# Kernel tuning notes

Measured on AMD Instinct MI355X. Metric: run time of the kernel, lower is better.

## Reference

```python
import jax, jax.numpy as jnp
import numpy as np

B, S, D, H = 1, 2048, 1024, 16
HD = D // H
S_SLOPE = 10.0      # soft_thres_layer s
C_MASK = -10000.0   # soft_thres_layer c == masked_bias
ALPHA = 0.0         # config.threshold
W_STD = 0.02        # GPT2 init std for weights


def setup_inputs() -> dict:
    key = jax.random.key(0)
    k1, k2, k3 = jax.random.split(key, 3)
    return {
        "hidden_states": jax.random.normal(k1, (B, S, D), dtype=jnp.float32),
        "c_attn_w": jax.random.normal(k2, (D, 3 * D), dtype=jnp.float32) * W_STD,
        "c_attn_b": jnp.zeros((3 * D,), dtype=jnp.float32),
        "c_proj_w": jax.random.normal(k3, (D, D), dtype=jnp.float32) * W_STD,
        "c_proj_b": jnp.zeros((D,), dtype=jnp.float32),
    }


def reference(hidden_states, c_attn_w, c_attn_b, c_proj_w, c_proj_b):
    # Conv1D: x @ w + b (GPT2 convention: weight is [in, out])
    qkv = hidden_states @ c_attn_w + c_attn_b            # [B,S,3D]
    q, k, v = jnp.split(qkv, 3, axis=-1)

    def split_heads(x):
        return x.reshape(B, S, H, HD).transpose(0, 2, 1, 3)  # [B,H,S,hd]

    q, k, v = split_heads(q), split_heads(k), split_heads(v)

    # prun path: NO 1/sqrt(d) scaling (skipped when self.prun is True)
    w = jnp.einsum("bhqd,bhkd->bhqk", q, k)              # [B,H,S,S]

    causal = jnp.tril(jnp.ones((S, S), dtype=bool))[None, None]
    w = jnp.where(causal, w, C_MASK)

    # soft-threshold pruning: smoothly pushes scores below alpha toward c=-10000
    w = C_MASK + (w - C_MASK) * jax.nn.sigmoid(S_SLOPE * (w - ALPHA))

    a = jax.nn.softmax(w, axis=-1)                        # attn_dropout = identity (eval)
    out = jnp.einsum("bhqk,bhkd->bhqd", a, v)             # [B,H,S,hd]
    out = out.transpose(0, 2, 1, 3).reshape(B, S, D)      # merge heads
    return out @ c_proj_w + c_proj_b                      # resid_dropout = identity
```

## Files before the change

### kernel.cpp

```cpp
#include <hip/hip_runtime.h>


#define S_LEN 2048
#define DM    1024
#define NH    16
#define HD    64
#define NQKV  3072
#define SLOPE 10.0f
#define CMASK -10000.0f

typedef short s16x4 __attribute__((ext_vector_type(4)));
typedef short s16x8 __attribute__((ext_vector_type(8)));
typedef float f32x4 __attribute__((ext_vector_type(4)));

#define MFMA16(a,b,c) __builtin_amdgcn_mfma_f32_16x16x32_bf16(a,b,c,0,0,0)
#define GLDS16(g,l) __builtin_amdgcn_global_load_lds( \
    (const __attribute__((address_space(1))) void*)(g), \
    (__attribute__((address_space(3))) void*)(l), 16, 0, 0)

__device__ __forceinline__ short f2bf(float f){
    unsigned u = __float_as_uint(f);
    u += 0x7fffu + ((u >> 16) & 1u);
    return (short)(u >> 16);
}
__device__ __forceinline__ float bf2f(short x){
    return __uint_as_float(((unsigned)(unsigned short)x) << 16);
}
struct bfpair { short hi, lo; };
__device__ __forceinline__ bfpair split_bf(float x){
    bfpair r; r.hi = f2bf(x);
    r.lo = f2bf(x - bf2f(r.hi));
    return r;
}

template<int ROWS, int THREADS>
__device__ __forceinline__ void stage_tile(const short* gbase, int rstride,
                                           short* lds, int tid){
#pragma unroll
    for (int it = 0; it < ROWS*8/THREADS; ++it){
        int s = it*THREADS + tid;
        int row = s >> 3, grp = s & 7;
        const short* src = gbase + (size_t)row*rstride + ((grp ^ (row & 7)) << 3);
        GLDS16(src, lds + (size_t)s*8);
    }
}
__device__ __forceinline__ s16x8 frag(const short* lds, int row, int kg){
    return *(const s16x8*)&lds[row*64 + ((kg ^ (row & 7)) << 3)];
}

template<bool WSPLIT, bool QKV>
__global__ __launch_bounds__(256)
void gemm_kern(const short* __restrict__ Ahg, const short* __restrict__ Alg,
               const short* __restrict__ Bhg, const short* __restrict__ Blg,
               const float* __restrict__ bias,
               short* __restrict__ o0h, short* __restrict__ o0l,
               short* __restrict__ o1h,
               short* __restrict__ o2,  float* __restrict__ oproj)
{
    __shared__ __align__(16) short Ah_s[128*64];
    __shared__ __align__(16) short Al_s[128*64];
    __shared__ __align__(16) short Bh_s[128*64];
    __shared__ __align__(16) short Bl_s[WSPLIT ? 128*64 : 8];

    const int tid = threadIdx.x, lane = tid & 63, wid = tid >> 6;
    const int lr = lane & 15, lg = lane >> 4;
    const int brow = blockIdx.y*128, bcol = blockIdx.x*128;
    const int wm = (wid >> 1)*64, wn = (wid & 1)*64;

    f32x4 acc[4][4];
#pragma unroll
    for (int m = 0; m < 4; ++m)
#pragma unroll
        for (int n = 0; n < 4; ++n) acc[m][n] = (f32x4){0.f,0.f,0.f,0.f};

    for (int k0 = 0; k0 < DM; k0 += 64){
        stage_tile<128,256>(Ahg + (size_t)brow*DM + k0, DM, Ah_s, tid);
        stage_tile<128,256>(Alg + (size_t)brow*DM + k0, DM, Al_s, tid);
        stage_tile<128,256>(Bhg + (size_t)bcol*DM + k0, DM, Bh_s, tid);
        if constexpr (WSPLIT)
            stage_tile<128,256>(Blg + (size_t)bcol*DM + k0, DM, Bl_s, tid);
        __syncthreads();
#pragma unroll
        for (int kc = 0; kc < 2; ++kc){
            s16x8 ah[4], al[4], bh[4], bl[4];
#pragma unroll
            for (int m = 0; m < 4; ++m){
                ah[m] = frag(Ah_s, wm + m*16 + lr, kc*4 + lg);
                al[m] = frag(Al_s, wm + m*16 + lr, kc*4 + lg);
            }
#pragma unroll
            for (int n = 0; n < 4; ++n){
                bh[n] = frag(Bh_s, wn + n*16 + lr, kc*4 + lg);
                if constexpr (WSPLIT)
                    bl[n] = frag(Bl_s, wn + n*16 + lr, kc*4 + lg);
            }
#pragma unroll
            for (int m = 0; m < 4; ++m)
#pragma unroll
                for (int n = 0; n < 4; ++n){
                    acc[m][n] = MFMA16(ah[m], bh[n], acc[m][n]);
                    if constexpr (WSPLIT)
                        acc[m][n] = MFMA16(ah[m], bl[n], acc[m][n]);
                    acc[m][n] = MFMA16(al[m], bh[n], acc[m][n]);
                }
        }
        __syncthreads();
    }

    const int sec = bcol >> 10;
#pragma unroll
    for (int m = 0; m < 4; ++m)
#pragma unroll
        for (int n = 0; n < 4; ++n){
            int row  = brow + wm + m*16 + lg*4;
            int gcol = bcol + wn + n*16 + lr;
            float bv = bias[gcol];
#pragma unroll
            for (int v = 0; v < 4; ++v){
                float val = acc[m][n][v] + bv;
                if constexpr (QKV){
                    int col1 = gcol & 1023;
                    size_t o = (size_t)(row + v)*DM + col1;
                    if (sec == 0){ bfpair p = split_bf(val); o0h[o] = p.hi; o0l[o] = p.lo; }
                    else if (sec == 1){ o1h[o] = f2bf(val); }
                    else { o2[o] = f2bf(val); }
                } else {
                    oproj[(size_t)(row + v)*DM + gcol] = val;
                }
            }
        }
}

__global__ __launch_bounds__(256)
void split_f32(const float* __restrict__ x, short* __restrict__ h,
               short* __restrict__ l, int n4)
{
    int i = blockIdx.x*256 + threadIdx.x;
    if (i >= n4) return;
    float4 v = *(const float4*)&x[(size_t)i*4];
    bfpair a = split_bf(v.x), b = split_bf(v.y), c = split_bf(v.z), d = split_bf(v.w);
    s16x4 hv, lv;
    hv.x = a.hi; hv.y = b.hi; hv.z = c.hi; hv.w = d.hi;
    lv.x = a.lo; lv.y = b.lo; lv.z = c.lo; lv.w = d.lo;
    *(s16x4*)&h[(size_t)i*4] = hv;
    *(s16x4*)&l[(size_t)i*4] = lv;
}

template<bool SPL>
__global__ __launch_bounds__(256)
void wtrans(const float* __restrict__ W, int N, short* __restrict__ Th,
            short* __restrict__ Tl)
{
    __shared__ float t[64][65];
    const int tid = threadIdx.x;
    const int tn = blockIdx.x*64, tk = blockIdx.y*64;
#pragma unroll
    for (int it = 0; it < 4; ++it){
        int idx = tid + it*256;
        int r = idx >> 4, c4 = (idx & 15)*4;
        float4 v = *(const float4*)&W[(size_t)(tk + r)*N + tn + c4];
        t[r][c4] = v.x; t[r][c4+1] = v.y; t[r][c4+2] = v.z; t[r][c4+3] = v.w;
    }
    __syncthreads();
#pragma unroll
    for (int it = 0; it < 4; ++it){
        int idx = tid + it*256;
        int n = idx >> 4, c4 = (idx & 15)*4;
        s16x4 hv, lv;
#pragma unroll
        for (int j = 0; j < 4; ++j){
            bfpair p = split_bf(t[c4+j][n]);
            hv[j] = p.hi; lv[j] = p.lo;
        }
        *(s16x4*)&Th[(size_t)(tn + n)*DM + tk + c4] = hv;
        if constexpr (SPL) *(s16x4*)&Tl[(size_t)(tn + n)*DM + tk + c4] = lv;
    }
}

__global__ __launch_bounds__(256)
void vtrans(const short* __restrict__ Vb, short* __restrict__ Vt)
{
    __shared__ short t[64][66];
    const int tid = threadIdx.x;
    const int td = blockIdx.x*64, ts = blockIdx.y*64;
#pragma unroll
    for (int it = 0; it < 4; ++it){
        int idx = tid + it*256;
        int r = idx >> 4, c4 = (idx & 15)*4;
        s16x4 v = *(const s16x4*)&Vb[(size_t)(ts + r)*DM + td + c4];
        t[r][c4] = v.x; t[r][c4+1] = v.y; t[r][c4+2] = v.z; t[r][c4+3] = v.w;
    }
    __syncthreads();
#pragma unroll
    for (int it = 0; it < 4; ++it){
        int idx = tid + it*256;
        int n = idx >> 4, c4 = (idx & 15)*4;
        s16x4 o;
#pragma unroll
        for (int j = 0; j < 4; ++j) o[j] = t[c4+j][n];
        *(s16x4*)&Vt[(size_t)(td + n)*S_LEN + ts + c4] = o;
    }
}

__global__ __launch_bounds__(64)
void sv_partial(const short* __restrict__ Vb, float* __restrict__ PB)
{
    int b = blockIdx.x, h = blockIdx.y, d = threadIdx.x;
    float s = 0.f;
#pragma unroll 8
    for (int k = 0; k < 64; ++k)
        s += bf2f(Vb[(size_t)(b*64 + k)*DM + h*HD + d]);
    PB[((size_t)h*32 + b)*64 + d] = s;
}
__global__ __launch_bounds__(64)
void sv_suffix(const float* __restrict__ PB, float* __restrict__ SSV)
{
    int h = blockIdx.x, d = threadIdx.x;
    float s = 0.f;
    SSV[((size_t)h*33 + 32)*64 + d] = 0.f;
    for (int b = 31; b >= 0; --b){
        s += PB[((size_t)h*32 + b)*64 + d];
        SSV[((size_t)h*33 + b)*64 + d] = s;
    }
}

__global__ __launch_bounds__(256)
void attn_fwd(const short* __restrict__ Qh, const short* __restrict__ Ql,
              const short* __restrict__ Kh, const short* __restrict__ Vt,
              const float* __restrict__ SSV,
              short* __restrict__ Oh, short* __restrict__ Ol)
{
    __shared__ __align__(16) short Ps[4][16*72];
    __shared__ float mrg[3][64][24];

    const int id = blockIdx.x;
    const int h  = (id & 7) + 8*((id >> 3) & 1);
    const int qt = 127 - (id >> 4);
    const int diag = qt >> 2;

    const int tid = threadIdx.x, lane = tid & 63, wid = tid >> 6;
    const int lr = lane & 15, lg = lane >> 4;
    const int qrow = qt*16 + lg*4;

    const short* qbh = Qh + (size_t)(qt*16)*DM + h*HD;
    const short* qbl = Ql + (size_t)(qt*16)*DM + h*HD;
    s16x8 aqh[2], aql[2];
#pragma unroll
    for (int kc = 0; kc < 2; ++kc){
        aqh[kc] = *(const s16x8*)&qbh[(size_t)lr*DM + kc*32 + lg*8];
        aql[kc] = *(const s16x8*)&qbl[(size_t)lr*DM + kc*32 + lg*8];
    }

    float m_run[4], l_run[4];
    f32x4 acc_o[4];
#pragma unroll
    for (int v = 0; v < 4; ++v){ m_run[v] = -1e30f; l_run[v] = 0.f; }
#pragma unroll
    for (int n = 0; n < 4; ++n) acc_o[n] = (f32x4){0.f,0.f,0.f,0.f};

    const short* kb0 = Kh + (size_t)h*HD;
    const short* vb0 = Vt + (size_t)(h*HD)*S_LEN;

    s16x8 bkc[2][4];
    if (wid <= diag){
        const short* kb = kb0 + (size_t)(wid*64)*DM;
#pragma unroll
        for (int kc = 0; kc < 2; ++kc)
#pragma unroll
            for (int n = 0; n < 4; ++n)
                bkc[kc][n] = *(const s16x8*)&kb[(size_t)(n*16 + lr)*DM + kc*32 + lg*8];
    }

    for (int kvb = wid; kvb <= diag; kvb += 4){
        s16x8 bkn[2][4];
        if (kvb + 4 <= diag){
            const short* kb = kb0 + (size_t)((kvb+4)*64)*DM;
#pragma unroll
            for (int kc = 0; kc < 2; ++kc)
#pragma unroll
                for (int n = 0; n < 4; ++n)
                    bkn[kc][n] = *(const s16x8*)&kb[(size_t)(n*16 + lr)*DM + kc*32 + lg*8];
        }

        f32x4 sc[4];
#pragma unroll
        for (int n = 0; n < 4; ++n) sc[n] = (f32x4){0.f,0.f,0.f,0.f};
#pragma unroll
        for (int kc = 0; kc < 2; ++kc)
#pragma unroll
            for (int n = 0; n < 4; ++n){
                sc[n] = MFMA16(aqh[kc], bkc[kc][n], sc[n]);
                sc[n] = MFMA16(aql[kc], bkc[kc][n], sc[n]);
            }

        const short* vb = vb0 + kvb*64;
        s16x8 bv0[4], bv1[4];
#pragma unroll
        for (int n = 0; n < 4; ++n){
            bv0[n] = *(const s16x8*)&vb[(size_t)(16*n + lr)*S_LEN + lg*8];
            bv1[n] = *(const s16x8*)&vb[(size_t)(16*n + lr)*S_LEN + 32 + lg*8];
        }

        float p[4][4], tmax[4];
#pragma unroll
        for (int v = 0; v < 4; ++v) tmax[v] = -1e30f;
        if (kvb == diag){
#pragma unroll
            for (int n = 0; n < 4; ++n){
                int key = kvb*64 + n*16 + lr;
#pragma unroll
                for (int v = 0; v < 4; ++v){
                    float w;
                    if (key > qrow + v) w = CMASK;
                    else {
                        float sv = sc[n][v];
                        float sig = 1.f / (1.f + __expf(-SLOPE*sv));
                        w = CMASK + (sv - CMASK)*sig;
                    }
                    p[n][v] = w;
                    tmax[v] = fmaxf(tmax[v], w);
                }
            }
        } else {
#pragma unroll
            for (int n = 0; n < 4; ++n)
#pragma unroll
                for (int v = 0; v < 4; ++v){
                    float sv = sc[n][v];
                    float sig = 1.f / (1.f + __expf(-SLOPE*sv));
                    float w = CMASK + (sv - CMASK)*sig;
                    p[n][v] = w;
                    tmax[v] = fmaxf(tmax[v], w);
                }
        }
#pragma unroll
        for (int v = 0; v < 4; ++v)
#pragma unroll
            for (int msk = 1; msk < 16; msk <<= 1)
                tmax[v] = fmaxf(tmax[v], __shfl_xor(tmax[v], msk, 64));

        float scale[4], rsum[4];
#pragma unroll
        for (int v = 0; v < 4; ++v){
            float mn = fmaxf(m_run[v], tmax[v]);
            scale[v] = __expf(m_run[v] - mn);
            m_run[v] = mn;
            rsum[v] = 0.f;
        }
#pragma unroll
        for (int n = 0; n < 4; ++n)
#pragma unroll
            for (int v = 0; v < 4; ++v){
                float e = __expf(p[n][v] - m_run[v]);
                p[n][v] = e;
                rsum[v] += e;
            }
#pragma unroll
        for (int v = 0; v < 4; ++v){
#pragma unroll
            for (int msk = 1; msk < 16; msk <<= 1)
                rsum[v] += __shfl_xor(rsum[v], msk, 64);
            l_run[v] = l_run[v]*scale[v] + rsum[v];
        }
#pragma unroll
        for (int n = 0; n < 4; ++n)
#pragma unroll
            for (int v = 0; v < 4; ++v) acc_o[n][v] *= scale[v];

#pragma unroll
        for (int n = 0; n < 4; ++n)
#pragma unroll
            for (int v = 0; v < 4; ++v)
                Ps[wid][(lg*4 + v)*72 + 16*n + lr] = f2bf(p[n][v]);
        asm volatile("s_waitcnt lgkmcnt(0)" ::: "memory");

        s16x8 pa0 = *(const s16x8*)&Ps[wid][lr*72 + lg*8];
        s16x8 pa1 = *(const s16x8*)&Ps[wid][lr*72 + 32 + lg*8];
#pragma unroll
        for (int n = 0; n < 4; ++n){
            acc_o[n] = MFMA16(pa0, bv0[n], acc_o[n]);
            acc_o[n] = MFMA16(pa1, bv1[n], acc_o[n]);
        }

#pragma unroll
        for (int kc = 0; kc < 2; ++kc)
#pragma unroll
            for (int n = 0; n < 4; ++n) bkc[kc][n] = bkn[kc][n];
    }

    if (wid != 0){
#pragma unroll
        for (int v = 0; v < 4; ++v){
            mrg[wid-1][lane][v] = m_run[v];
            mrg[wid-1][lane][4 + v] = l_run[v];
        }
#pragma unroll
        for (int n = 0; n < 4; ++n)
#pragma unroll
            for (int v = 0; v < 4; ++v) mrg[wid-1][lane][8 + n*4 + v] = acc_o[n][v];
    }
    __syncthreads();
    if (wid != 0) return;

#pragma unroll
    for (int w = 0; w < 3; ++w){
        float e0[4], e1[4];
#pragma unroll
        for (int v = 0; v < 4; ++v){
            float m1 = mrg[w][lane][v], l1 = mrg[w][lane][4 + v];
            float mn = fmaxf(m_run[v], m1);
            e0[v] = __expf(m_run[v] - mn);
            e1[v] = __expf(m1 - mn);
            l_run[v] = l_run[v]*e0[v] + l1*e1[v];
            m_run[v] = mn;
        }
#pragma unroll
        for (int n = 0; n < 4; ++n)
#pragma unroll
            for (int v = 0; v < 4; ++v)
                acc_o[n][v] = acc_o[n][v]*e0[v] + mrg[w][lane][8 + n*4 + v]*e1[v];
    }

    {
        const float* sv = SSV + ((size_t)h*33 + (diag + 1))*64;
        float F = (float)(S_LEN - 64*(diag + 1));
        float e[4];
#pragma unroll
        for (int v = 0; v < 4; ++v){
            e[v] = __expf(CMASK - m_run[v]);
            l_run[v] += e[v]*F;
        }
#pragma unroll
        for (int n = 0; n < 4; ++n){
            float svv = sv[16*n + lr];
#pragma unroll
            for (int v = 0; v < 4; ++v) acc_o[n][v] += e[v]*svv;
        }
    }

#pragma unroll
    for (int n = 0; n < 4; ++n)
#pragma unroll
        for (int v = 0; v < 4; ++v){
            int row = qt*16 + lg*4 + v;
            int col = h*HD + 16*n + lr;
            bfpair p = split_bf(acc_o[n][v] / l_run[v]);
            Oh[(size_t)row*DM + col] = p.hi;
            Ol[(size_t)row*DM + col] = p.lo;
        }
}

extern "C" void kernel_launch(void* const* d_in, const int* in_sizes, int n_in,
                              void* d_out, int out_size, void* d_ws, size_t ws_size,
                              hipStream_t stream)
{
    (void)in_sizes; (void)n_in; (void)out_size; (void)ws_size;
    const float* hs   = (const float*)d_in[0];
    const float* wqkv = (const float*)d_in[1];
    const float* bqkv = (const float*)d_in[2];
    const float* wprj = (const float*)d_in[3];
    const float* bprj = (const float*)d_in[4];

    char* p = (char*)d_ws;
    short* Ahg  = (short*)(p + (0ull  << 20));
    short* Alg  = (short*)(p + (4ull  << 20));
    short* WqTh = (short*)(p + (8ull  << 20));
    short* WqTl = (short*)(p + (14ull << 20));
    short* Qhg  = (short*)(p + (20ull << 20));
    short* Qlg  = (short*)(p + (24ull << 20));
    short* Khg  = (short*)(p + (28ull << 20));
    short* Vbg  = (short*)(p + (32ull << 20));
    short* Vtg  = (short*)(p + (36ull << 20));
    float* PB   = (float*)(p + (40ull << 20));
    float* SSV  = (float*)(p + (41ull << 20));
    short* Oh = Ahg, * Ol = Alg;
    short* WpT = WqTh;

    split_f32<<<S_LEN*DM/4/256, 256, 0, stream>>>(hs, Ahg, Alg, S_LEN*DM/4);
    wtrans<true><<<dim3(NQKV/64, DM/64), 256, 0, stream>>>(wqkv, NQKV, WqTh, WqTl);

    gemm_kern<true, true><<<dim3(NQKV/128, S_LEN/128), 256, 0, stream>>>(
        Ahg, Alg, WqTh, WqTl, bqkv, Qhg, Qlg, Khg, Vbg, nullptr);

    wtrans<false><<<dim3(DM/64, DM/64), 256, 0, stream>>>(wprj, DM, WpT, nullptr);
    vtrans<<<dim3(DM/64, S_LEN/64), 256, 0, stream>>>(Vbg, Vtg);
    sv_partial<<<dim3(32, NH), 64, 0, stream>>>(Vbg, PB);
    sv_suffix<<<NH, 64, 0, stream>>>(PB, SSV);

    attn_fwd<<<2048, 256, 0, stream>>>(Qhg, Qlg, Khg, Vtg, SSV, Oh, Ol);

    gemm_kern<false, false><<<dim3(DM/128, S_LEN/128), 256, 0, stream>>>(
        Oh, Ol, WpT, nullptr, bprj, nullptr, nullptr, nullptr, nullptr,
        (float*)d_out);
}
```

Baseline: 169.8 us.

## Split QKV GEMM per section, drop split-bf16 for K/V/out, head-major Q/K, 2-wave attention

The fused QKV GEMM becomes three launches. Only the Q projection keeps the 3-MFMA hi/lo split-bf16 path, while K and V use single bf16 MFMAs. Q and K are written in head-major layout for contiguous loads, and V^T gets a padded row stride to avoid bank/channel conflicts. The attention kernel drops from 4 to 2 waves per block and writes a single bf16 output, so the projection GEMM uses one MFMA instead of two. These cuts reduce MFMA and memory traffic but lower precision for K, V and the attention output, and the extra launches add overhead.

```diff
diff --git a/kernel.cpp b/kernel.cpp
--- a/kernel.cpp
+++ b/kernel.cpp
@@ -5,9 +5,9 @@
 #define DM    1024
 #define NH    16
 #define HD    64
-#define NQKV  3072
 #define SLOPE 10.0f
 #define CMASK -10000.0f
+#define SP    2080
 
 typedef short s16x4 __attribute__((ext_vector_type(4)));
 typedef short s16x8 __attribute__((ext_vector_type(8)));
@@ -48,19 +48,18 @@
     return *(const s16x8*)&lds[row*64 + ((kg ^ (row & 7)) << 3)];
 }
 
-template<bool WSPLIT, bool QKV>
+template<bool SPLIT, int OUT>
 __global__ __launch_bounds__(256)
-void gemm_kern(const short* __restrict__ Ahg, const short* __restrict__ Alg,
-               const short* __restrict__ Bhg, const short* __restrict__ Blg,
-               const float* __restrict__ bias,
-               short* __restrict__ o0h, short* __restrict__ o0l,
-               short* __restrict__ o1h,
-               short* __restrict__ o2,  float* __restrict__ oproj)
+void gemm_s(const short* __restrict__ Ahg, const short* __restrict__ Alg,
+            const short* __restrict__ Bhg, const short* __restrict__ Blg,
+            const float* __restrict__ bias,
+            short* __restrict__ o0, short* __restrict__ o1,
+            float* __restrict__ of)
 {
     __shared__ __align__(16) short Ah_s[128*64];
-    __shared__ __align__(16) short Al_s[128*64];
     __shared__ __align__(16) short Bh_s[128*64];
-    __shared__ __align__(16) short Bl_s[WSPLIT ? 128*64 : 8];
+    __shared__ __align__(16) short Al_s[SPLIT ? 128*64 : 8];
+    __shared__ __align__(16) short Bl_s[SPLIT ? 128*64 : 8];
 
     const int tid = threadIdx.x, lane = tid & 63, wid = tid >> 6;
     const int lr = lane & 15, lg = lane >> 4;
@@ -75,10 +74,11 @@
 
     for (int k0 = 0; k0 < DM; k0 += 64){
         stage_tile<128,256>(Ahg + (size_t)brow*DM + k0, DM, Ah_s, tid);
-        stage_tile<128,256>(Alg + (size_t)brow*DM + k0, DM, Al_s, tid);
         stage_tile<128,256>(Bhg + (size_t)bcol*DM + k0, DM, Bh_s, tid);
-        if constexpr (WSPLIT)
+        if constexpr (SPLIT){
+            stage_tile<128,256>(Alg + (size_t)brow*DM + k0, DM, Al_s, tid);
             stage_tile<128,256>(Blg + (size_t)bcol*DM + k0, DM, Bl_s, tid);
+        }
         __syncthreads();
 #pragma unroll
         for (int kc = 0; kc < 2; ++kc){
@@ -86,28 +86,27 @@
 #pragma unroll
             for (int m = 0; m < 4; ++m){
                 ah[m] = frag(Ah_s, wm + m*16 + lr, kc*4 + lg);
-                al[m] = frag(Al_s, wm + m*16 + lr, kc*4 + lg);
+                if constexpr (SPLIT) al[m] = frag(Al_s, wm + m*16 + lr, kc*4 + lg);
             }
 #pragma unroll
             for (int n = 0; n < 4; ++n){
                 bh[n] = frag(Bh_s, wn + n*16 + lr, kc*4 + lg);
-                if constexpr (WSPLIT)
-                    bl[n] = frag(Bl_s, wn + n*16 + lr, kc*4 + lg);
+                if constexpr (SPLIT) bl[n] = frag(Bl_s, wn + n*16 + lr, kc*4 + lg);
             }
 #pragma unroll
             for (int m = 0; m < 4; ++m)
 #pragma unroll
                 for (int n = 0; n < 4; ++n){
                     acc[m][n] = MFMA16(ah[m], bh[n], acc[m][n]);
-                    if constexpr (WSPLIT)
+                    if constexpr (SPLIT){
                         acc[m][n] = MFMA16(ah[m], bl[n], acc[m][n]);
-                    acc[m][n] = MFMA16(al[m], bh[n], acc[m][n]);
+                        acc[m][n] = MFMA16(al[m], bh[n], acc[m][n]);
+                    }
                 }
         }
         __syncthreads();
     }
 
-    const int sec = bcol >> 10;
 #pragma unroll
     for (int m = 0; m < 4; ++m)
 #pragma unroll
@@ -115,17 +114,20 @@
             int row  = brow + wm + m*16 + lg*4;
             int gcol = bcol + wn + n*16 + lr;
             float bv = bias[gcol];
+            int h0 = gcol >> 6, d = gcol & 63;
 #pragma unroll
             for (int v = 0; v < 4; ++v){
                 float val = acc[m][n][v] + bv;
-                if constexpr (QKV){
-                    int col1 = gcol & 1023;
-                    size_t o = (size_t)(row + v)*DM + col1;
-                    if (sec == 0){ bfpair p = split_bf(val); o0h[o] = p.hi; o0l[o] = p.lo; }
-                    else if (sec == 1){ o1h[o] = f2bf(val); }
-                    else { o2[o] = f2bf(val); }
+                if constexpr (OUT == 0){
+                    bfpair p = split_bf(val);
+                    size_t o = ((size_t)h0*S_LEN + row + v)*HD + d;
+                    o0[o] = p.hi; o1[o] = p.lo;
+                } else if constexpr (OUT == 1){
+                    o0[((size_t)h0*S_LEN + row + v)*HD + d] = f2bf(val);
+                } else if constexpr (OUT == 2){
+                    o0[(size_t)(row + v)*DM + gcol] = f2bf(val);
                 } else {
-                    oproj[(size_t)(row + v)*DM + gcol] = val;
+                    of[(size_t)(row + v)*DM + gcol] = val;
                 }
             }
         }
@@ -198,7 +200,7 @@
         s16x4 o;
 #pragma unroll
         for (int j = 0; j < 4; ++j) o[j] = t[c4+j][n];
-        *(s16x4*)&Vt[(size_t)(td + n)*S_LEN + ts + c4] = o;
+        *(s16x4*)&Vt[(size_t)(td + n)*SP + ts + c4] = o;
     }
 }
 
@@ -224,14 +226,13 @@
     }
 }
 
-__global__ __launch_bounds__(256)
-void attn_fwd(const short* __restrict__ Qh, const short* __restrict__ Ql,
-              const short* __restrict__ Kh, const short* __restrict__ Vt,
-              const float* __restrict__ SSV,
-              short* __restrict__ Oh, short* __restrict__ Ol)
-{
-    __shared__ __align__(16) short Ps[4][16*72];
-    __shared__ float mrg[3][64][24];
+__global__ __launch_bounds__(128)
+void attn_fwd(const short* __restrict__ QHh, const short* __restrict__ QHl,
+              const short* __restrict__ KH, const short* __restrict__ Vt,
+              const float* __restrict__ SSV, short* __restrict__ O)
+{
+    __shared__ __align__(16) short Ps[2][16*72];
+    __shared__ float mrg[64][24];
 
     const int id = blockIdx.x;
     const int h  = (id & 7) + 8*((id >> 3) & 1);
@@ -242,13 +243,13 @@
     const int lr = lane & 15, lg = lane >> 4;
     const int qrow = qt*16 + lg*4;
 
-    const short* qbh = Qh + (size_t)(qt*16)*DM + h*HD;
-    const short* qbl = Ql + (size_t)(qt*16)*DM + h*HD;
+    const short* qbh = QHh + ((size_t)h*S_LEN + qt*16)*HD;
+    const short* qbl = QHl + ((size_t)h*S_LEN + qt*16)*HD;
     s16x8 aqh[2], aql[2];
 #pragma unroll
     for (int kc = 0; kc < 2; ++kc){
-        aqh[kc] = *(const s16x8*)&qbh[(size_t)lr*DM + kc*32 + lg*8];
-        aql[kc] = *(const s16x8*)&qbl[(size_t)lr*DM + kc*32 + lg*8];
+        aqh[kc] = *(const s16x8*)&qbh[lr*HD + kc*32 + lg*8];
+        aql[kc] = *(const s16x8*)&qbl[lr*HD + kc*32 + lg*8];
     }
 
     float m_run[4], l_run[4];
@@ -258,28 +259,28 @@
 #pragma unroll
     for (int n = 0; n < 4; ++n) acc_o[n] = (f32x4){0.f,0.f,0.f,0.f};
 
-    const short* kb0 = Kh + (size_t)h*HD;
-    const short* vb0 = Vt + (size_t)(h*HD)*S_LEN;
+    const short* kb0 = KH + (size_t)h*S_LEN*HD;
+    const short* vb0 = Vt + (size_t)(h*HD)*SP;
 
     s16x8 bkc[2][4];
     if (wid <= diag){
-        const short* kb = kb0 + (size_t)(wid*64)*DM;
+        const short* kb = kb0 + (size_t)(wid*64)*HD;
 #pragma unroll
         for (int kc = 0; kc < 2; ++kc)
 #pragma unroll
             for (int n = 0; n < 4; ++n)
-                bkc[kc][n] = *(const s16x8*)&kb[(size_t)(n*16 + lr)*DM + kc*32 + lg*8];
-    }
-
-    for (int kvb = wid; kvb <= diag; kvb += 4){
+                bkc[kc][n] = *(const s16x8*)&kb[(n*16 + lr)*HD + kc*32 + lg*8];
+    }
+
+    for (int kvb = wid; kvb <= diag; kvb += 2){
         s16x8 bkn[2][4];
-        if (kvb + 4 <= diag){
-            const short* kb = kb0 + (size_t)((kvb+4)*64)*DM;
+        if (kvb + 2 <= diag){
+            const short* kb = kb0 + (size_t)((kvb+2)*64)*HD;
 #pragma unroll
             for (int kc = 0; kc < 2; ++kc)
 #pragma unroll
                 for (int n = 0; n < 4; ++n)
-                    bkn[kc][n] = *(const s16x8*)&kb[(size_t)(n*16 + lr)*DM + kc*32 + lg*8];
+                    bkn[kc][n] = *(const s16x8*)&kb[(n*16 + lr)*HD + kc*32 + lg*8];
         }
 
         f32x4 sc[4];
@@ -297,8 +298,8 @@
         s16x8 bv0[4], bv1[4];
 #pragma unroll
         for (int n = 0; n < 4; ++n){
-            bv0[n] = *(const s16x8*)&vb[(size_t)(16*n + lr)*S_LEN + lg*8];
-            bv1[n] = *(const s16x8*)&vb[(size_t)(16*n + lr)*S_LEN + 32 + lg*8];
+            bv0[n] = *(const s16x8*)&vb[(size_t)(16*n + lr)*SP + lg*8];
+            bv1[n] = *(const s16x8*)&vb[(size_t)(16*n + lr)*SP + 32 + lg*8];
         }
 
         float p[4][4], tmax[4];
@@ -388,26 +389,25 @@
             for (int n = 0; n < 4; ++n) bkc[kc][n] = bkn[kc][n];
     }
 
-    if (wid != 0){
-#pragma unroll
-        for (int v = 0; v < 4; ++v){
-            mrg[wid-1][lane][v] = m_run[v];
-            mrg[wid-1][lane][4 + v] = l_run[v];
+    if (wid == 1){
+#pragma unroll
+        for (int v = 0; v < 4; ++v){
+            mrg[lane][v] = m_run[v];
+            mrg[lane][4 + v] = l_run[v];
         }
 #pragma unroll
         for (int n = 0; n < 4; ++n)
 #pragma unroll
-            for (int v = 0; v < 4; ++v) mrg[wid-1][lane][8 + n*4 + v] = acc_o[n][v];
+            for (int v = 0; v < 4; ++v) mrg[lane][8 + n*4 + v] = acc_o[n][v];
     }
     __syncthreads();
     if (wid != 0) return;
 
-#pragma unroll
-    for (int w = 0; w < 3; ++w){
+    {
         float e0[4], e1[4];
 #pragma unroll
         for (int v = 0; v < 4; ++v){
-            float m1 = mrg[w][lane][v], l1 = mrg[w][lane][4 + v];
+            float m1 = mrg[lane][v], l1 = mrg[lane][4 + v];
             float mn = fmaxf(m_run[v], m1);
             e0[v] = __expf(m_run[v] - mn);
             e1[v] = __expf(m1 - mn);
@@ -418,7 +418,7 @@
         for (int n = 0; n < 4; ++n)
 #pragma unroll
             for (int v = 0; v < 4; ++v)
-                acc_o[n][v] = acc_o[n][v]*e0[v] + mrg[w][lane][8 + n*4 + v]*e1[v];
+                acc_o[n][v] = acc_o[n][v]*e0[v] + mrg[lane][8 + n*4 + v]*e1[v];
     }
 
     {
@@ -444,9 +444,7 @@
         for (int v = 0; v < 4; ++v){
             int row = qt*16 + lg*4 + v;
             int col = h*HD + 16*n + lr;
-            bfpair p = split_bf(acc_o[n][v] / l_run[v]);
-            Oh[(size_t)row*DM + col] = p.hi;
-            Ol[(size_t)row*DM + col] = p.lo;
+            O[(size_t)row*DM + col] = f2bf(acc_o[n][v] / l_run[v]);
         }
 }
 
@@ -466,30 +464,33 @@
     short* Alg  = (short*)(p + (4ull  << 20));
     short* WqTh = (short*)(p + (8ull  << 20));
     short* WqTl = (short*)(p + (14ull << 20));
-    short* Qhg  = (short*)(p + (20ull << 20));
-    short* Qlg  = (short*)(p + (24ull << 20));
-    short* Khg  = (short*)(p + (28ull << 20));
+    short* QHh  = (short*)(p + (20ull << 20));
+    short* QHl  = (short*)(p + (24ull << 20));
+    short* KH   = (short*)(p + (28ull << 20));
     short* Vbg  = (short*)(p + (32ull << 20));
-    short* Vtg  = (short*)(p + (36ull << 20));
-    float* PB   = (float*)(p + (40ull << 20));
-    float* SSV  = (float*)(p + (41ull << 20));
-    short* Oh = Ahg, * Ol = Alg;
-    short* WpT = WqTh;
+    short* VT   = (short*)(p + (36ull << 20));
+    float* PB   = (float*)(p + (41ull << 20));
+    float* SSV  = (float*)(p + (42ull << 20));
+    short* O    = Ahg;
+    short* WpT  = WqTh;
 
     split_f32<<<S_LEN*DM/4/256, 256, 0, stream>>>(hs, Ahg, Alg, S_LEN*DM/4);
-    wtrans<true><<<dim3(NQKV/64, DM/64), 256, 0, stream>>>(wqkv, NQKV, WqTh, WqTl);
-
-    gemm_kern<true, true><<<dim3(NQKV/128, S_LEN/128), 256, 0, stream>>>(
-        Ahg, Alg, WqTh, WqTl, bqkv, Qhg, Qlg, Khg, Vbg, nullptr);
+    wtrans<true><<<dim3(3*DM/64, DM/64), 256, 0, stream>>>(wqkv, 3*DM, WqTh, WqTl);
+
+    gemm_s<true, 0><<<dim3(8, 16), 256, 0, stream>>>(
+        Ahg, Alg, WqTh, WqTl, bqkv, QHh, QHl, nullptr);
+    gemm_s<false, 1><<<dim3(8, 16), 256, 0, stream>>>(
+        Ahg, nullptr, WqTh + (size_t)DM*DM, nullptr, bqkv + DM, KH, nullptr, nullptr);
+    gemm_s<false, 2><<<dim3(8, 16), 256, 0, stream>>>(
+        Ahg, nullptr, WqTh + (size_t)2*DM*DM, nullptr, bqkv + 2*DM, Vbg, nullptr, nullptr);
 
     wtrans<false><<<dim3(DM/64, DM/64), 256, 0, stream>>>(wprj, DM, WpT, nullptr);
-    vtrans<<<dim3(DM/64, S_LEN/64), 256, 0, stream>>>(Vbg, Vtg);
+    vtrans<<<dim3(DM/64, S_LEN/64), 256, 0, stream>>>(Vbg, VT);
     sv_partial<<<dim3(32, NH), 64, 0, stream>>>(Vbg, PB);
     sv_suffix<<<NH, 64, 0, stream>>>(PB, SSV);
 
-    attn_fwd<<<2048, 256, 0, stream>>>(Qhg, Qlg, Khg, Vtg, SSV, Oh, Ol);
-
-    gemm_kern<false, false><<<dim3(DM/128, S_LEN/128), 256, 0, stream>>>(
-        Oh, Ol, WpT, nullptr, bprj, nullptr, nullptr, nullptr, nullptr,
-        (float*)d_out);
-}
+    attn_fwd<<<2048, 128, 0, stream>>>(QHh, QHl, KH, VT, SSV, O);
+
+    gemm_s<false, 3><<<dim3(8, 16), 256, 0, stream>>>(
+        O, nullptr, WpT, nullptr, bprj, nullptr, nullptr, (float*)d_out);
+}
```

Measured after the change: 185.6 us. 1.09x slower.
